# Optimization experiments

Hardware: AMD Instinct MI355X
Metric: run time of the kernel (lower is better)

The kernel has to match this reference:

```python
import jax, jax.numpy as jnp
import numpy as np

N_SINKHORN_ITERS = 20
SINKHORN_EPS = 1e-08  # also used as eps for the dynamic-H RMS norm (per docstring)
RMSNORM_EPS = 1e-05
ALPHA_INIT = 0.01
B, N_STREAMS, C = 4096, 4, 4096


def sinkhorn_knopp(M, num_iters=N_SINKHORN_ITERS, eps=SINKHORN_EPS):
    # Iterative row/column normalization toward a doubly-stochastic matrix.
    def body(i, M):
        M = M / (jnp.sum(M, axis=-1, keepdims=True) + eps)
        M = M / (jnp.sum(M, axis=-2, keepdims=True) + eps)
        return M
    return jax.lax.fori_loop(0, num_iters, body, M)


def setup_inputs() -> dict:
    key = jax.random.key(0)
    ks = jax.random.split(key, 4)
    n, nC = N_STREAMS, N_STREAMS * C
    return {
        "x": jax.random.normal(ks[0], (B, n, C), dtype=jnp.float32),
        "rmsnorm_weight": jnp.ones((C,), dtype=jnp.float32),
        "phi_pre": jax.random.normal(ks[1], (n, nC), dtype=jnp.float32) * 0.02,
        "phi_post": jax.random.normal(ks[2], (n, nC), dtype=jnp.float32) * 0.02,
        "phi_res": jax.random.normal(ks[3], (n * n, nC), dtype=jnp.float32) * 0.02,
        "b_pre": jnp.zeros((n,), dtype=jnp.float32),
        "b_post": jnp.zeros((n,), dtype=jnp.float32),
        "b_res": jnp.zeros((n, n), dtype=jnp.float32),
        "alpha_pre": jnp.float32(ALPHA_INIT),
        "alpha_post": jnp.float32(ALPHA_INIT),
        "alpha_res": jnp.float32(ALPHA_INIT),
    }


def reference(x, rmsnorm_weight, phi_pre, phi_post, phi_res,
              b_pre, b_post, b_res, alpha_pre, alpha_post, alpha_res):
    Bd, n, Cd = x.shape
    # --- dynamic H projections from RMS-normalized flattened streams ---
    xf = x.reshape(Bd, n * Cd)                                   # [B, nC]
    xn = xf * jax.lax.rsqrt(jnp.mean(xf * xf, axis=-1, keepdims=True) + SINKHORN_EPS)
    h_pre = alpha_pre * (xn @ phi_pre.T) + b_pre                 # [B, n]
    h_post = alpha_post * (xn @ phi_post.T) + b_post             # [B, n]
    h_res = (alpha_res * (xn @ phi_res.T)).reshape(Bd, n, n) + b_res  # [B, n, n]
    # --- manifold constraints ---
    H_pre = jax.nn.softmax(h_pre, axis=-1)                       # simplex (aggregation weights)
    H_post = 2.0 * jax.nn.sigmoid(h_post)                        # gain in (0, 2), ~1 at init
    M = sinkhorn_knopp(jnp.exp(h_res))                           # doubly-stochastic mixing [B, n, n]
    # --- aggregate -> rmsnorm -> distribute + mix + add ---
    x_agg = jnp.einsum('bn,bnc->bc', H_pre, x)                   # [B, C]
    y_norm = x_agg * jax.lax.rsqrt(jnp.mean(x_agg * x_agg, axis=-1, keepdims=True) + RMSNORM_EPS)
    y_norm = y_norm * rmsnorm_weight
    out = H_post[..., None] * y_norm[:, None, :] + jnp.einsum('bij,bjc->bic', M, x)
    return out
```

## Files before the change

### kernel.cpp

```cpp
#include <hip/hip_runtime.h>
#include <math.h>

#define B_ROWS 4096
#define NSTR 4
#define C_DIM 4096
#define NC 16384
#define NC4 4096
#define C4 1024

#define ASYNC_COPY16(g, l)                                                     \
    __builtin_amdgcn_global_load_lds(                                         \
        (const __attribute__((address_space(1))) void*)(g),                   \
        (__attribute__((address_space(3))) void*)(l), 16, 0, 0)

__global__ void repack_kernel(
    const float4* __restrict__ pre4,
    const float4* __restrict__ post4,
    const float4* __restrict__ res4,
    float4* __restrict__ phiws4)
{
    const int idx = blockIdx.x * blockDim.x + threadIdx.x;
    if (idx >= 24 * NC4) return;
    const int row = idx / NC4;
    const int k4  = idx % NC4;
    float4 v;
    if (row < 4)        v = pre4[row * NC4 + k4];
    else if (row < 8)   v = post4[(row - 4) * NC4 + k4];
    else                v = res4[(row - 8) * NC4 + k4];
    phiws4[idx] = v;
}

__global__ __launch_bounds__(512, 4) void proj_kernel(
    const float* __restrict__ x,
    const float* __restrict__ phiws,
    float* __restrict__ dots_part)
{
    const float4* __restrict__ x4   = reinterpret_cast<const float4*>(x);
    const float4* __restrict__ phi4 = reinterpret_cast<const float4*>(phiws);

    const int bid  = blockIdx.x;
    const int kb   = bid & 1;
    const int b0   = (bid >> 1) * 8;
    const int wave = threadIdx.x >> 6;
    const int lane = threadIdx.x & 63;
    const int wv   = __builtin_amdgcn_readfirstlane(wave);

    __shared__ float4 xs[2][8][256];
    __shared__ float  red[8][8][3];
    __shared__ float  redss[8];

    const int kbase = kb * 2048;

    const float4* __restrict__ srcw    = x4 + (size_t)(b0 + wave) * NC4 + kbase + lane;
    const float4* __restrict__ phibase = phi4 + (size_t)(wave * 3) * NC4 + kbase + lane;

    float acc[8][3];
#pragma unroll
    for (int r = 0; r < 8; ++r)
#pragma unroll
        for (int j = 0; j < 3; ++j) acc[r][j] = 0.f;
    float ssq = 0.f;

#pragma unroll
    for (int i = 0; i < 4; ++i)
        ASYNC_COPY16(srcw + i * 64, &xs[0][wave][i * 64]);
    __syncthreads();

    int cur = 0;
#pragma unroll 1
    for (int c = 0; c < 8; ++c) {
        if (c < 7) {
#pragma unroll
            for (int i = 0; i < 4; ++i)
                ASYNC_COPY16(srcw + (c + 1) * 256 + i * 64,
                             &xs[cur ^ 1][wave][i * 64]);
        }

        const float4* __restrict__ pb = phibase + c * 256;
#pragma unroll 1
        for (int u = 0; u < 4; ++u) {
            const int ki = u * 64 + lane;

            const float4 p0 = pb[(size_t)0 * NC4 + u * 64];
            const float4 p1 = pb[(size_t)1 * NC4 + u * 64];
            const float4 p2 = pb[(size_t)2 * NC4 + u * 64];

            const float4 xw = xs[cur][wv][ki];
            ssq += xw.x*xw.x + xw.y*xw.y + xw.z*xw.z + xw.w*xw.w;

#pragma unroll
            for (int r = 0; r < 8; ++r) {
                const float4 xv = xs[cur][r][ki];
                acc[r][0] += xv.x*p0.x + xv.y*p0.y + xv.z*p0.z + xv.w*p0.w;
                acc[r][1] += xv.x*p1.x + xv.y*p1.y + xv.z*p1.z + xv.w*p1.w;
                acc[r][2] += xv.x*p2.x + xv.y*p2.y + xv.z*p2.z + xv.w*p2.w;
            }
        }

        __syncthreads();
        cur ^= 1;
    }

#pragma unroll
    for (int r = 0; r < 8; ++r)
#pragma unroll
        for (int j = 0; j < 3; ++j) {
            float v = acc[r][j];
#pragma unroll
            for (int off = 32; off > 0; off >>= 1)
                v += __shfl_xor(v, off, 64);
            acc[r][j] = v;
        }
#pragma unroll
    for (int off = 32; off > 0; off >>= 1)
        ssq += __shfl_xor(ssq, off, 64);

    if (lane == 0) {
#pragma unroll
        for (int r = 0; r < 8; ++r)
#pragma unroll
            for (int j = 0; j < 3; ++j)
                red[wave][r][j] = acc[r][j];
        redss[wave] = ssq;
    }
    __syncthreads();

    const int t = threadIdx.x;
    if (t < 200) {
        const int r = t / 25, o = t % 25;
        float s;
        if (o < 24) s = red[o / 3][r][o % 3];
        else        s = redss[r];
        dots_part[((size_t)kb * B_ROWS + (b0 + r)) * 25 + o] = s;
    }
}

__global__ void finalize_kernel(
    const float* __restrict__ dots_part,
    const float* __restrict__ b_pre,
    const float* __restrict__ b_post,
    const float* __restrict__ b_res,
    const float* __restrict__ alpha_pre,
    const float* __restrict__ alpha_post,
    const float* __restrict__ alpha_res,
    float* __restrict__ params)
{
    const int row = blockIdx.x * blockDim.x + threadIdx.x;
    if (row >= B_ROWS) return;

    const float* d0 = dots_part + (size_t)row * 25;
    const float* d1 = dots_part + ((size_t)B_ROWS + row) * 25;
    float d[25];
#pragma unroll
    for (int o = 0; o < 25; ++o) d[o] = d0[o] + d1[o];

    const float inv_rms = rsqrtf(d[24] * (1.f / (float)NC) + 1e-8f);
    const float ap  = alpha_pre[0];
    const float apo = alpha_post[0];
    const float ar  = alpha_res[0];

    float hp[4];
    float mx = -1e30f;
#pragma unroll
    for (int j = 0; j < 4; ++j) {
        hp[j] = ap * d[j] * inv_rms + b_pre[j];
        mx = fmaxf(mx, hp[j]);
    }
    float e[4], s = 0.f;
#pragma unroll
    for (int j = 0; j < 4; ++j) { e[j] = expf(hp[j] - mx); s += e[j]; }
    float Hpre[4];
#pragma unroll
    for (int j = 0; j < 4; ++j) Hpre[j] = e[j] / s;

    float Hpost[4];
#pragma unroll
    for (int j = 0; j < 4; ++j) {
        const float h = apo * d[4 + j] * inv_rms + b_post[j];
        Hpost[j] = 2.f / (1.f + expf(-h));
    }

    float M[16];
#pragma unroll
    for (int k = 0; k < 16; ++k)
        M[k] = expf(ar * d[8 + k] * inv_rms + b_res[k]);

    for (int it = 0; it < 20; ++it) {
#pragma unroll
        for (int i = 0; i < 4; ++i) {
            const float rs = M[i*4+0] + M[i*4+1] + M[i*4+2] + M[i*4+3] + 1e-8f;
#pragma unroll
            for (int j = 0; j < 4; ++j) M[i*4+j] = M[i*4+j] / rs;
        }
#pragma unroll
        for (int j = 0; j < 4; ++j) {
            const float cs = M[0*4+j] + M[1*4+j] + M[2*4+j] + M[3*4+j] + 1e-8f;
#pragma unroll
            for (int i = 0; i < 4; ++i) M[i*4+j] = M[i*4+j] / cs;
        }
    }

    float* p = params + (size_t)row * 24;
#pragma unroll
    for (int j = 0; j < 4; ++j)  p[j]     = Hpre[j];
#pragma unroll
    for (int j = 0; j < 4; ++j)  p[4 + j] = Hpost[j];
#pragma unroll
    for (int k = 0; k < 16; ++k) p[8 + k] = M[k];
}

__global__ __launch_bounds__(256, 2) void out_kernel(
    const float* __restrict__ x,
    const float* __restrict__ w,
    const float* __restrict__ params,
    float* __restrict__ out)
{
    const float4* __restrict__ x4 = reinterpret_cast<const float4*>(x);
    const float4* __restrict__ w4 = reinterpret_cast<const float4*>(w);
    float4* __restrict__ out4 = reinterpret_cast<float4*>(out);

    const int b = blockIdx.x;
    const float* __restrict__ p = params + (size_t)b * 24;

    float Hpre[4], Hpost[4], M[16];
#pragma unroll
    for (int j = 0; j < 4; ++j)  Hpre[j]  = p[j];
#pragma unroll
    for (int j = 0; j < 4; ++j)  Hpost[j] = p[4 + j];
#pragma unroll
    for (int k = 0; k < 16; ++k) M[k]     = p[8 + k];

    const int t = threadIdx.x;
    const size_t base = (size_t)b * NC4;

    float4 xv[4][4];
    float4 agg[4];
    float ssq = 0.f;

#pragma unroll
    for (int u = 0; u < 4; ++u) {
        const int c4 = u * 256 + t;
#pragma unroll
        for (int n = 0; n < 4; ++n)
            xv[u][n] = x4[base + (size_t)n * C4 + c4];

        float4 a;
        a.x = Hpre[0]*xv[u][0].x + Hpre[1]*xv[u][1].x + Hpre[2]*xv[u][2].x + Hpre[3]*xv[u][3].x;
        a.y = Hpre[0]*xv[u][0].y + Hpre[1]*xv[u][1].y + Hpre[2]*xv[u][2].y + Hpre[3]*xv[u][3].y;
        a.z = Hpre[0]*xv[u][0].z + Hpre[1]*xv[u][1].z + Hpre[2]*xv[u][2].z + Hpre[3]*xv[u][3].z;
        a.w = Hpre[0]*xv[u][0].w + Hpre[1]*xv[u][1].w + Hpre[2]*xv[u][2].w + Hpre[3]*xv[u][3].w;
        agg[u] = a;
        ssq += a.x*a.x + a.y*a.y + a.z*a.z + a.w*a.w;
    }

#pragma unroll
    for (int off = 32; off > 0; off >>= 1)
        ssq += __shfl_xor(ssq, off, 64);
    __shared__ float red[4];
    if ((t & 63) == 0) red[t >> 6] = ssq;
    __syncthreads();
    const float total = red[0] + red[1] + red[2] + red[3];
    const float inv = rsqrtf(total * (1.f / (float)C_DIM) + 1e-5f);

#pragma unroll
    for (int u = 0; u < 4; ++u) {
        const int c4 = u * 256 + t;
        const float4 wv = w4[c4];
        float4 y;
        y.x = agg[u].x * inv * wv.x;
        y.y = agg[u].y * inv * wv.y;
        y.z = agg[u].z * inv * wv.z;
        y.w = agg[u].w * inv * wv.w;

#pragma unroll
        for (int i = 0; i < 4; ++i) {
            float4 o;
            o.x = Hpost[i]*y.x + M[i*4+0]*xv[u][0].x + M[i*4+1]*xv[u][1].x
                               + M[i*4+2]*xv[u][2].x + M[i*4+3]*xv[u][3].x;
            o.y = Hpost[i]*y.y + M[i*4+0]*xv[u][0].y + M[i*4+1]*xv[u][1].y
                               + M[i*4+2]*xv[u][2].y + M[i*4+3]*xv[u][3].y;
            o.z = Hpost[i]*y.z + M[i*4+0]*xv[u][0].z + M[i*4+1]*xv[u][1].z
                               + M[i*4+2]*xv[u][2].z + M[i*4+3]*xv[u][3].z;
            o.w = Hpost[i]*y.w + M[i*4+0]*xv[u][0].w + M[i*4+1]*xv[u][1].w
                               + M[i*4+2]*xv[u][2].w + M[i*4+3]*xv[u][3].w;
            out4[base + (size_t)i * C4 + c4] = o;
        }
    }
}

extern "C" void kernel_launch(void* const* d_in, const int* in_sizes, int n_in,
                              void* d_out, int out_size, void* d_ws, size_t ws_size,
                              hipStream_t stream) {
    const float* x        = (const float*)d_in[0];
    const float* w        = (const float*)d_in[1];
    const float* phi_pre  = (const float*)d_in[2];
    const float* phi_post = (const float*)d_in[3];
    const float* phi_res  = (const float*)d_in[4];
    const float* b_pre    = (const float*)d_in[5];
    const float* b_post   = (const float*)d_in[6];
    const float* b_res    = (const float*)d_in[7];
    const float* a_pre    = (const float*)d_in[8];
    const float* a_post   = (const float*)d_in[9];
    const float* a_res    = (const float*)d_in[10];
    float* out = (float*)d_out;

    float* dots_part = (float*)d_ws;
    float* params    = dots_part + (size_t)2 * B_ROWS * 25;
    float* phiws     = params + (size_t)B_ROWS * 24;

    hipLaunchKernelGGL(repack_kernel, dim3((24 * NC4 + 255) / 256), dim3(256), 0, stream,
                       (const float4*)phi_pre, (const float4*)phi_post,
                       (const float4*)phi_res, (float4*)phiws);
    hipLaunchKernelGGL(proj_kernel, dim3(B_ROWS / 4), dim3(512), 0, stream,
                       x, phiws, dots_part);
    hipLaunchKernelGGL(finalize_kernel, dim3(B_ROWS / 256), dim3(256), 0, stream,
                       dots_part, b_pre, b_post, b_res, a_pre, a_post, a_res, params);
    hipLaunchKernelGGL(out_kernel, dim3(B_ROWS), dim3(256), 0, stream,
                       x, w, params, out);
}
```

Before: 228.3 us.

## Halve proj_kernel waves, give each wave six phi rows and two x rows

```diff
diff --git a/kernel.cpp b/kernel.cpp
--- a/kernel.cpp
+++ b/kernel.cpp
@@ -30,7 +30,7 @@
     phiws4[idx] = v;
 }
 
-__global__ __launch_bounds__(512, 4) void proj_kernel(
+__global__ __launch_bounds__(256, 4) void proj_kernel(
     const float* __restrict__ x,
     const float* __restrict__ phiws,
     float* __restrict__ dots_part)
@@ -44,56 +44,76 @@
     const int wave = threadIdx.x >> 6;
     const int lane = threadIdx.x & 63;
     const int wv   = __builtin_amdgcn_readfirstlane(wave);
-
-    __shared__ float4 xs[2][8][256];
-    __shared__ float  red[8][8][3];
+    const int wr0  = 2 * wv;
+    const int wr1  = 2 * wv + 1;
+
+    __shared__ float4 xs[2][8][128];
+    __shared__ float  red[4][8][6];
     __shared__ float  redss[8];
 
     const int kbase = kb * 2048;
 
-    const float4* __restrict__ srcw    = x4 + (size_t)(b0 + wave) * NC4 + kbase + lane;
-    const float4* __restrict__ phibase = phi4 + (size_t)(wave * 3) * NC4 + kbase + lane;
-
-    float acc[8][3];
+    const float4* __restrict__ srcA = x4 + (size_t)(b0 + 2 * wave)     * NC4 + kbase + lane;
+    const float4* __restrict__ srcB = x4 + (size_t)(b0 + 2 * wave + 1) * NC4 + kbase + lane;
+    const float4* __restrict__ phibase = phi4 + (size_t)(wave * 6) * NC4 + kbase + lane;
+
+    float acc[8][6];
 #pragma unroll
     for (int r = 0; r < 8; ++r)
 #pragma unroll
-        for (int j = 0; j < 3; ++j) acc[r][j] = 0.f;
-    float ssq = 0.f;
-
-#pragma unroll
-    for (int i = 0; i < 4; ++i)
-        ASYNC_COPY16(srcw + i * 64, &xs[0][wave][i * 64]);
+        for (int j = 0; j < 6; ++j) acc[r][j] = 0.f;
+    float ssq0 = 0.f, ssq1 = 0.f;
+
+    ASYNC_COPY16(srcA,      &xs[0][2 * wave][0]);
+    ASYNC_COPY16(srcA + 64, &xs[0][2 * wave][64]);
+    ASYNC_COPY16(srcB,      &xs[0][2 * wave + 1][0]);
+    ASYNC_COPY16(srcB + 64, &xs[0][2 * wave + 1][64]);
     __syncthreads();
 
     int cur = 0;
 #pragma unroll 1
-    for (int c = 0; c < 8; ++c) {
-        if (c < 7) {
-#pragma unroll
-            for (int i = 0; i < 4; ++i)
-                ASYNC_COPY16(srcw + (c + 1) * 256 + i * 64,
-                             &xs[cur ^ 1][wave][i * 64]);
-        }
-
-        const float4* __restrict__ pb = phibase + c * 256;
+    for (int c = 0; c < 16; ++c) {
+        if (c < 15) {
+            const int nf = (c + 1) * 128;
+            ASYNC_COPY16(srcA + nf,      &xs[cur ^ 1][2 * wave][0]);
+            ASYNC_COPY16(srcA + nf + 64, &xs[cur ^ 1][2 * wave][64]);
+            ASYNC_COPY16(srcB + nf,      &xs[cur ^ 1][2 * wave + 1][0]);
+            ASYNC_COPY16(srcB + nf + 64, &xs[cur ^ 1][2 * wave + 1][64]);
+        }
+
+        const float4* __restrict__ pb = phibase + c * 128;
 #pragma unroll 1
-        for (int u = 0; u < 4; ++u) {
+        for (int u = 0; u < 2; ++u) {
             const int ki = u * 64 + lane;
 
-            const float4 p0 = pb[(size_t)0 * NC4 + u * 64];
-            const float4 p1 = pb[(size_t)1 * NC4 + u * 64];
-            const float4 p2 = pb[(size_t)2 * NC4 + u * 64];
-
-            const float4 xw = xs[cur][wv][ki];
-            ssq += xw.x*xw.x + xw.y*xw.y + xw.z*xw.z + xw.w*xw.w;
+            float4 p[6];
+#pragma unroll
+            for (int j = 0; j < 6; ++j)
+                p[j] = pb[(size_t)j * NC4 + u * 64];
 
 #pragma unroll
             for (int r = 0; r < 8; ++r) {
                 const float4 xv = xs[cur][r][ki];
-                acc[r][0] += xv.x*p0.x + xv.y*p0.y + xv.z*p0.z + xv.w*p0.w;
-                acc[r][1] += xv.x*p1.x + xv.y*p1.y + xv.z*p1.z + xv.w*p1.w;
-                acc[r][2] += xv.x*p2.x + xv.y*p2.y + xv.z*p2.z + xv.w*p2.w;
+#pragma unroll
+                for (int j = 0; j < 6; ++j) {
+                    float a = acc[r][j];
+                    a = fmaf(xv.x, p[j].x, a);
+                    a = fmaf(xv.y, p[j].y, a);
+                    a = fmaf(xv.z, p[j].z, a);
+                    a = fmaf(xv.w, p[j].w, a);
+                    acc[r][j] = a;
+                }
+                if (r == wr0) {
+                    ssq0 = fmaf(xv.x, xv.x, ssq0);
+                    ssq0 = fmaf(xv.y, xv.y, ssq0);
+                    ssq0 = fmaf(xv.z, xv.z, ssq0);
+                    ssq0 = fmaf(xv.w, xv.w, ssq0);
+                } else if (r == wr1) {
+                    ssq1 = fmaf(xv.x, xv.x, ssq1);
+                    ssq1 = fmaf(xv.y, xv.y, ssq1);
+                    ssq1 = fmaf(xv.z, xv.z, ssq1);
+                    ssq1 = fmaf(xv.w, xv.w, ssq1);
+                }
             }
         }
 
@@ -104,7 +124,7 @@
 #pragma unroll
     for (int r = 0; r < 8; ++r)
 #pragma unroll
-        for (int j = 0; j < 3; ++j) {
+        for (int j = 0; j < 6; ++j) {
             float v = acc[r][j];
 #pragma unroll
             for (int off = 32; off > 0; off >>= 1)
@@ -113,15 +133,19 @@
         }
 #pragma unroll
     for (int off = 32; off > 0; off >>= 1)
-        ssq += __shfl_xor(ssq, off, 64);
+        ssq0 += __shfl_xor(ssq0, off, 64);
+#pragma unroll
+    for (int off = 32; off > 0; off >>= 1)
+        ssq1 += __shfl_xor(ssq1, off, 64);
 
     if (lane == 0) {
 #pragma unroll
         for (int r = 0; r < 8; ++r)
 #pragma unroll
-            for (int j = 0; j < 3; ++j)
+            for (int j = 0; j < 6; ++j)
                 red[wave][r][j] = acc[r][j];
-        redss[wave] = ssq;
+        redss[2 * wave]     = ssq0;
+        redss[2 * wave + 1] = ssq1;
     }
     __syncthreads();
 
@@ -129,7 +153,7 @@
     if (t < 200) {
         const int r = t / 25, o = t % 25;
         float s;
-        if (o < 24) s = red[o / 3][r][o % 3];
+        if (o < 24) s = red[o / 6][r][o % 6];
         else        s = redss[r];
         dots_part[((size_t)kb * B_ROWS + (b0 + r)) * 25 + o] = s;
     }
@@ -311,7 +335,7 @@
     hipLaunchKernelGGL(repack_kernel, dim3((24 * NC4 + 255) / 256), dim3(256), 0, stream,
                        (const float4*)phi_pre, (const float4*)phi_post,
                        (const float4*)phi_res, (float4*)phiws);
-    hipLaunchKernelGGL(proj_kernel, dim3(B_ROWS / 4), dim3(512), 0, stream,
+    hipLaunchKernelGGL(proj_kernel, dim3(B_ROWS / 4), dim3(256), 0, stream,
                        x, phiws, dots_part);
     hipLaunchKernelGGL(finalize_kernel, dim3(B_ROWS / 256), dim3(256), 0, stream,
                        dots_part, b_pre, b_post, b_res, a_pre, a_post, a_res, params);
```

Result: faster. 217.7 us (-4.6%).
